# Kernel tuning notes

Hardware: AMD Instinct MI355X
Metric: run time of the kernel (lower is better)

The kernel has to match this reference:

```python
import jax, jax.numpy as jnp
import numpy as np

EPS = 1e-12
BETA = 0.25

def normalise(x, axis=-1):
    return x * jax.lax.rsqrt(jnp.mean(x * x, axis=axis, keepdims=True) + EPS)

def setup_inputs() -> dict:
    key = jax.random.key(0)
    ks = jax.random.split(key, 4)
    N, F, D, C = 8192, 512, 64, 8192
    return {
        "z": jax.random.normal(ks[0], (N, F), dtype=jnp.float32),
        "W_in": jax.random.normal(ks[1], (F, D), dtype=jnp.float32) * (1.0 / np.sqrt(F)),
        "b_in": jnp.zeros((D,), dtype=jnp.float32),
        "codebook": jax.random.normal(ks[2], (C, D), dtype=jnp.float32),
        "W_out": jax.random.normal(ks[3], (D, F), dtype=jnp.float32) * (1.0 / np.sqrt(D)),
        "b_out": jnp.zeros((F,), dtype=jnp.float32),
    }

def reference(z, W_in, b_in, codebook, W_out, b_out):
    sg = jax.lax.stop_gradient
    # input projection: [N, F] -> [N, D]
    zp = z @ W_in + b_in
    zn = normalise(zp)                  # [N, D]
    cn = normalise(codebook)            # [C, D]
    # squared euclidean distance via matmul expansion (same math as
    # sum((z[:,None]-c[None])**2, -1), avoids [N,C,D] materialization)
    z_sq = jnp.sum(zn * zn, axis=-1, keepdims=True)          # [N, 1]
    c_sq = jnp.sum(cn * cn, axis=-1)[None, :]                # [1, C]
    distance = z_sq + c_sq - 2.0 * (zn @ cn.T)               # [N, C]
    idxes = jnp.argmin(distance, axis=-1)                    # [N]
    codes = normalise(codebook[idxes], axis=-1)               # [N, D]
    loss = BETA * jnp.mean((sg(zn) - codes) ** 2) + jnp.mean((zn - sg(codes)) ** 2)
    codes = zn + sg(codes - zn)                               # straight-through
    out = codes @ W_out + b_out                               # [N, F]
    return (out, loss, idxes)
```

## Files before the change

kernel.cpp:

```cpp
#include <hip/hip_runtime.h>
#include <hip/hip_bf16.h>

#define N_ROWS 8192
#define F_DIM  512
#define D_DIM  64
#define C_CODES 8192

typedef __attribute__((ext_vector_type(8))) short bf16x8;
typedef __attribute__((ext_vector_type(4))) float f32x4;

__device__ __forceinline__ unsigned short rne_bf16(float x) {
  unsigned u = __float_as_uint(x);
  return (unsigned short)((u + 0x7FFFu + ((u >> 16) & 1u)) >> 16);
}
__device__ __forceinline__ float bf16_to_f(unsigned short u) {
  return __uint_as_float(((unsigned)u) << 16);
}
__device__ __forceinline__ void limb3(const float* xs, bf16x8& H, bf16x8& M, bf16x8& L) {
  #pragma unroll
  for (int j = 0; j < 8; ++j) {
    float x = xs[j];
    unsigned short h = rne_bf16(x);
    float r1 = x - bf16_to_f(h);
    unsigned short m = rne_bf16(r1);
    float r2 = r1 - bf16_to_f(m);
    unsigned short lo = rne_bf16(r2);
    H[j] = (short)h; M[j] = (short)m; L[j] = (short)lo;
  }
}

__global__ __launch_bounds__(256) void k_swz_win(
    const float* __restrict__ W, unsigned short* __restrict__ dst) {
  const int tid = threadIdx.x, w = tid >> 6, l = tid & 63;
  const int task = blockIdx.x * 4 + w;
  const int kc = task >> 2, cg = task & 3;
  const int lo = l & 15, hi = l >> 4;
  float xs[8];
  #pragma unroll
  for (int j = 0; j < 8; ++j)
    xs[j] = W[(size_t)(kc * 32 + hi * 8 + j) * D_DIM + cg * 16 + lo];
  bf16x8 H, M, L;
  limb3(xs, H, M, L);
  const int fb = (kc * 4 + cg) * 3;
  unsigned short* d0 = dst + (size_t)(fb + 0) * 512 + l * 8;
  unsigned short* d1 = dst + (size_t)(fb + 1) * 512 + l * 8;
  unsigned short* d2 = dst + (size_t)(fb + 2) * 512 + l * 8;
  #pragma unroll
  for (int j = 0; j < 8; ++j) { d0[j] = (unsigned short)H[j]; d1[j] = (unsigned short)M[j]; d2[j] = (unsigned short)L[j]; }
}

__global__ __launch_bounds__(256) void k_swz_wout(
    const float* __restrict__ W, unsigned short* __restrict__ dst) {
  const int tid = threadIdx.x, w = tid >> 6, l = tid & 63;
  const int task = blockIdx.x * 4 + w;
  const int cg = task >> 1, c = task & 1;
  const int lo = l & 15, hi = l >> 4;
  float xs[8];
  #pragma unroll
  for (int j = 0; j < 8; ++j)
    xs[j] = W[(size_t)(c * 32 + hi * 8 + j) * F_DIM + cg * 16 + lo];
  bf16x8 H, M, L;
  limb3(xs, H, M, L);
  const int fb = (cg * 2 + c) * 3;
  unsigned short* d0 = dst + (size_t)(fb + 0) * 512 + l * 8;
  unsigned short* d1 = dst + (size_t)(fb + 1) * 512 + l * 8;
  unsigned short* d2 = dst + (size_t)(fb + 2) * 512 + l * 8;
  #pragma unroll
  for (int j = 0; j < 8; ++j) { d0[j] = (unsigned short)H[j]; d1[j] = (unsigned short)M[j]; d2[j] = (unsigned short)L[j]; }
}

__global__ __launch_bounds__(256) void k_cn(
    const float* __restrict__ cb, float* __restrict__ cn,
    unsigned short* __restrict__ cn_sw) {
  const int tid = threadIdx.x, w = tid >> 6, l = tid & 63;
  const int g = blockIdx.x * 4 + w;
  const int lo = l & 15, hi = l >> 4;
  const int code = g * 16 + lo;

  float xs[2][8];
  float s = 0.0f;
  #pragma unroll
  for (int c = 0; c < 2; ++c) {
    const float* sp = cb + (size_t)code * D_DIM + c * 32 + hi * 8;
    float4 a = *(const float4*)sp, b = *(const float4*)(sp + 4);
    xs[c][0]=a.x; xs[c][1]=a.y; xs[c][2]=a.z; xs[c][3]=a.w;
    xs[c][4]=b.x; xs[c][5]=b.y; xs[c][6]=b.z; xs[c][7]=b.w;
    #pragma unroll
    for (int j = 0; j < 8; ++j) s += xs[c][j] * xs[c][j];
  }
  s += __shfl_xor(s, 16);
  s += __shfl_xor(s, 32);
  float inv = rsqrtf(s * (1.0f / 64.0f) + 1e-12f);

  #pragma unroll
  for (int c = 0; c < 2; ++c) {
    #pragma unroll
    for (int j = 0; j < 8; ++j) xs[c][j] *= inv;
    float* dp = cn + (size_t)code * D_DIM + c * 32 + hi * 8;
    *(float4*)dp = make_float4(xs[c][0], xs[c][1], xs[c][2], xs[c][3]);
    *(float4*)(dp + 4) = make_float4(xs[c][4], xs[c][5], xs[c][6], xs[c][7]);
    bf16x8 H, M, L;
    limb3(xs[c], H, M, L);
    const int fb = (g * 2 + c) * 3;
    unsigned short* d0 = cn_sw + (size_t)(fb + 0) * 512 + l * 8;
    unsigned short* d1 = cn_sw + (size_t)(fb + 1) * 512 + l * 8;
    unsigned short* d2 = cn_sw + (size_t)(fb + 2) * 512 + l * 8;
    #pragma unroll
    for (int j = 0; j < 8; ++j) { d0[j] = (unsigned short)H[j]; d1[j] = (unsigned short)M[j]; d2[j] = (unsigned short)L[j]; }
  }
}

__global__ __launch_bounds__(64) void k_zn(
    const float* __restrict__ z, const unsigned short* __restrict__ w_in_sw,
    const float* __restrict__ b_in, float* __restrict__ zn,
    unsigned short* __restrict__ zn_sw) {
  __shared__ float t_lds[16 * 65];
  const int l = threadIdx.x;
  const int lo = l & 15, hi = l >> 4;
  const int g = blockIdx.x;
  const int r0 = g * 16;
  const bf16x8* Bptr = (const bf16x8*)w_in_sw;
  const float* zbase = z + (size_t)(r0 + lo) * F_DIM + hi * 8;

  f32x4 acc[4];
  #pragma unroll
  for (int cg = 0; cg < 4; ++cg) acc[cg] = (f32x4){0.f, 0.f, 0.f, 0.f};

  bf16x8 Bu[12], Bv[12];
  #pragma unroll
  for (int i = 0; i < 12; ++i) Bu[i] = Bptr[(size_t)i * 64 + l];
  float4 za = *(const float4*)zbase;
  float4 zb = *(const float4*)(zbase + 4);

  #define ZSTEP(BCUR, BNXT, KC)                                               \
    {                                                                         \
      int kn = ((KC) < 15) ? (KC) + 1 : 15;                                   \
      float4 na = *(const float4*)(zbase + kn * 32);                          \
      float4 nb = *(const float4*)(zbase + kn * 32 + 4);                      \
      _Pragma("unroll")                                                       \
      for (int i = 0; i < 12; ++i)                                            \
        BNXT[i] = Bptr[((size_t)kn * 12 + i) * 64 + l];                       \
      float xs[8] = {za.x, za.y, za.z, za.w, zb.x, zb.y, zb.z, zb.w};         \
      bf16x8 Ah, Am, Al;                                                      \
      limb3(xs, Ah, Am, Al);                                                  \
      _Pragma("unroll")                                                       \
      for (int cg = 0; cg < 4; ++cg) {                                        \
        f32x4 t = acc[cg];                                                    \
        t = __builtin_amdgcn_mfma_f32_16x16x32_bf16(Ah, BCUR[cg*3+0], t, 0,0,0); \
        t = __builtin_amdgcn_mfma_f32_16x16x32_bf16(Ah, BCUR[cg*3+1], t, 0,0,0); \
        t = __builtin_amdgcn_mfma_f32_16x16x32_bf16(Am, BCUR[cg*3+0], t, 0,0,0); \
        t = __builtin_amdgcn_mfma_f32_16x16x32_bf16(Ah, BCUR[cg*3+2], t, 0,0,0); \
        t = __builtin_amdgcn_mfma_f32_16x16x32_bf16(Al, BCUR[cg*3+0], t, 0,0,0); \
        t = __builtin_amdgcn_mfma_f32_16x16x32_bf16(Am, BCUR[cg*3+1], t, 0,0,0); \
        acc[cg] = t;                                                          \
      }                                                                       \
      za = na; zb = nb;                                                       \
    }

  for (int kc = 0; kc < 16; kc += 2) {
    ZSTEP(Bu, Bv, kc)
    ZSTEP(Bv, Bu, kc + 1)
  }
  #undef ZSTEP

  #pragma unroll
  for (int r = 0; r < 4; ++r) {
    float v[4], s = 0.0f;
    #pragma unroll
    for (int cg = 0; cg < 4; ++cg) {
      v[cg] = acc[cg][r] + b_in[cg * 16 + lo];
      s += v[cg] * v[cg];
    }
    s += __shfl_xor(s, 1);
    s += __shfl_xor(s, 2);
    s += __shfl_xor(s, 4);
    s += __shfl_xor(s, 8);
    float inv = rsqrtf(s * (1.0f / 64.0f) + 1e-12f);
    #pragma unroll
    for (int cg = 0; cg < 4; ++cg)
      t_lds[(hi * 4 + r) * 65 + cg * 16 + lo] = v[cg] * inv;
  }
  __syncthreads();

  #pragma unroll
  for (int c = 0; c < 2; ++c) {
    float xs[8];
    #pragma unroll
    for (int j = 0; j < 8; ++j) xs[j] = t_lds[lo * 65 + c * 32 + hi * 8 + j];
    float* dp = zn + (size_t)(r0 + lo) * D_DIM + c * 32 + hi * 8;
    *(float4*)dp = make_float4(xs[0], xs[1], xs[2], xs[3]);
    *(float4*)(dp + 4) = make_float4(xs[4], xs[5], xs[6], xs[7]);
    bf16x8 H, M, L;
    limb3(xs, H, M, L);
    const int fb = (g * 2 + c) * 3;
    unsigned short* d0 = zn_sw + (size_t)(fb + 0) * 512 + l * 8;
    unsigned short* d1 = zn_sw + (size_t)(fb + 1) * 512 + l * 8;
    unsigned short* d2 = zn_sw + (size_t)(fb + 2) * 512 + l * 8;
    #pragma unroll
    for (int j = 0; j < 8; ++j) { d0[j] = (unsigned short)H[j]; d1[j] = (unsigned short)M[j]; d2[j] = (unsigned short)L[j]; }
  }
}

__global__ __launch_bounds__(256, 2) void k_argmax(
    const unsigned short* __restrict__ zn_sw,
    const unsigned short* __restrict__ cn_sw,
    float* __restrict__ pval, int* __restrict__ pidx) {
  const int tid = threadIdx.x;
  const int w = tid >> 6, l = tid & 63;
  const int lo = l & 15, hi = l >> 4;
  const int gA0 = (blockIdx.x * 4 + w) * 2;
  const int gB0 = blockIdx.y * 64;
  const bf16x8* Ab = (const bf16x8*)zn_sw;
  const bf16x8* Bb = (const bf16x8*)cn_sw;

  bf16x8 A0[2][3], A1[2][3];
  #pragma unroll
  for (int c = 0; c < 2; ++c)
    #pragma unroll
    for (int m = 0; m < 3; ++m) {
      A0[c][m] = Ab[(size_t)((gA0 * 2 + c) * 3 + m) * 64 + l];
      A1[c][m] = Ab[(size_t)(((gA0 + 1) * 2 + c) * 3 + m) * 64 + l];
    }

  bf16x8 Bu[2][3], Bv[2][3];
  #pragma unroll
  for (int c = 0; c < 2; ++c)
    #pragma unroll
    for (int m = 0; m < 3; ++m)
      Bu[c][m] = Bb[(size_t)((gB0 * 2 + c) * 3 + m) * 64 + l];

  float bv[8];
  int bi[8];
  #pragma unroll
  for (int i = 0; i < 8; ++i) { bv[i] = -1e30f; bi[i] = 0; }
  int cand = blockIdx.y * 1024 + lo;

  #define LOADB(dst, gB)                                                     \
    _Pragma("unroll")                                                        \
    for (int c = 0; c < 2; ++c)                                              \
      _Pragma("unroll")                                                      \
      for (int m = 0; m < 3; ++m)                                            \
        dst[c][m] = Bb[(size_t)(((gB) * 2 + c) * 3 + m) * 64 + l];

  #define COMPUTE(B)                                                          \
    {                                                                         \
      f32x4 a0 = {0.f,0.f,0.f,0.f}, a1 = {0.f,0.f,0.f,0.f};                   \
      f32x4 a2 = {0.f,0.f,0.f,0.f}, a3 = {0.f,0.f,0.f,0.f};                   \
      a0 = __builtin_amdgcn_mfma_f32_16x16x32_bf16(A0[0][0], B[0][0], a0, 0,0,0); \
      a1 = __builtin_amdgcn_mfma_f32_16x16x32_bf16(A0[1][0], B[1][0], a1, 0,0,0); \
      a2 = __builtin_amdgcn_mfma_f32_16x16x32_bf16(A1[0][0], B[0][0], a2, 0,0,0); \
      a3 = __builtin_amdgcn_mfma_f32_16x16x32_bf16(A1[1][0], B[1][0], a3, 0,0,0); \
      a0 = __builtin_amdgcn_mfma_f32_16x16x32_bf16(A0[0][0], B[0][1], a0, 0,0,0); \
      a1 = __builtin_amdgcn_mfma_f32_16x16x32_bf16(A0[1][0], B[1][1], a1, 0,0,0); \
      a2 = __builtin_amdgcn_mfma_f32_16x16x32_bf16(A1[0][0], B[0][1], a2, 0,0,0); \
      a3 = __builtin_amdgcn_mfma_f32_16x16x32_bf16(A1[1][0], B[1][1], a3, 0,0,0); \
      a0 = __builtin_amdgcn_mfma_f32_16x16x32_bf16(A0[0][1], B[0][0], a0, 0,0,0); \
      a1 = __builtin_amdgcn_mfma_f32_16x16x32_bf16(A0[1][1], B[1][0], a1, 0,0,0); \
      a2 = __builtin_amdgcn_mfma_f32_16x16x32_bf16(A1[0][1], B[0][0], a2, 0,0,0); \
      a3 = __builtin_amdgcn_mfma_f32_16x16x32_bf16(A1[1][1], B[1][0], a3, 0,0,0); \
      a0 = __builtin_amdgcn_mfma_f32_16x16x32_bf16(A0[0][0], B[0][2], a0, 0,0,0); \
      a1 = __builtin_amdgcn_mfma_f32_16x16x32_bf16(A0[1][0], B[1][2], a1, 0,0,0); \
      a2 = __builtin_amdgcn_mfma_f32_16x16x32_bf16(A1[0][0], B[0][2], a2, 0,0,0); \
      a3 = __builtin_amdgcn_mfma_f32_16x16x32_bf16(A1[1][0], B[1][2], a3, 0,0,0); \
      a0 = __builtin_amdgcn_mfma_f32_16x16x32_bf16(A0[0][2], B[0][0], a0, 0,0,0); \
      a1 = __builtin_amdgcn_mfma_f32_16x16x32_bf16(A0[1][2], B[1][0], a1, 0,0,0); \
      a2 = __builtin_amdgcn_mfma_f32_16x16x32_bf16(A1[0][2], B[0][0], a2, 0,0,0); \
      a3 = __builtin_amdgcn_mfma_f32_16x16x32_bf16(A1[1][2], B[1][0], a3, 0,0,0); \
      a0 = __builtin_amdgcn_mfma_f32_16x16x32_bf16(A0[0][1], B[0][1], a0, 0,0,0); \
      a1 = __builtin_amdgcn_mfma_f32_16x16x32_bf16(A0[1][1], B[1][1], a1, 0,0,0); \
      a2 = __builtin_amdgcn_mfma_f32_16x16x32_bf16(A1[0][1], B[0][1], a2, 0,0,0); \
      a3 = __builtin_amdgcn_mfma_f32_16x16x32_bf16(A1[1][1], B[1][1], a3, 0,0,0); \
      _Pragma("unroll")                                                       \
      for (int r = 0; r < 4; ++r) {                                           \
        float d0 = a0[r] + a1[r];                                             \
        if (d0 > bv[r]) { bv[r] = d0; bi[r] = cand; }                         \
        float d1 = a2[r] + a3[r];                                             \
        if (d1 > bv[4 + r]) { bv[4 + r] = d1; bi[4 + r] = cand; }             \
      }                                                                       \
      cand += 16;                                                             \
    }

  for (int p = 0; p < 64; p += 2) {
    LOADB(Bv, gB0 + p + 1);
    COMPUTE(Bu);
    LOADB(Bu, gB0 + p + 2);
    COMPUTE(Bv);
  }
  #undef LOADB
  #undef COMPUTE

  #pragma unroll
  for (int i = 0; i < 8; ++i) {
    float v = bv[i]; int ix = bi[i];
    #pragma unroll
    for (int m = 1; m < 16; m <<= 1) {
      float ov = __shfl_xor(v, m);
      int oi = __shfl_xor(ix, m);
      if (ov > v || (ov == v && oi < ix)) { v = ov; ix = oi; }
    }
    bv[i] = v; bi[i] = ix;
  }
  if (lo == 0) {
    int off = blockIdx.y * N_ROWS;
    int base0 = gA0 * 16 + hi * 4;
    int base1 = (gA0 + 1) * 16 + hi * 4;
    #pragma unroll
    for (int r = 0; r < 4; ++r) {
      pval[off + base0 + r] = bv[r];     pidx[off + base0 + r] = bi[r];
      pval[off + base1 + r] = bv[4 + r]; pidx[off + base1 + r] = bi[4 + r];
    }
  }
}

__global__ __launch_bounds__(64) void k_out(
    const float* __restrict__ cn, const float* __restrict__ zn,
    const float* __restrict__ pval, const int* __restrict__ pidx,
    const unsigned short* __restrict__ w_out_sw,
    const float* __restrict__ b_out, float* __restrict__ out,
    float* __restrict__ idx_f, float* __restrict__ pl) {
  const int l = threadIdx.x;
  const int lo = l & 15, hi = l >> 4;
  const int r0 = blockIdx.x * 16;
  const int row = r0 + lo;

  float v = pval[row];
  int ix = pidx[row];
  #pragma unroll
  for (int q = 1; q < 8; ++q) {
    float vq = pval[q * N_ROWS + row];
    int iq = pidx[q * N_ROWS + row];
    if (vq > v) { v = vq; ix = iq; }
  }
  if (hi == 0) idx_f[row] = (float)ix;

  bf16x8 A[2][3];
  float lp = 0.0f;
  #pragma unroll
  for (int c = 0; c < 2; ++c) {
    const float* cp = cn + (size_t)ix * D_DIM + c * 32 + hi * 8;
    const float* zp = zn + (size_t)row * D_DIM + c * 32 + hi * 8;
    float4 c0 = *(const float4*)cp, c1 = *(const float4*)(cp + 4);
    float4 z0 = *(const float4*)zp, z1 = *(const float4*)(zp + 4);
    float xs[8] = {c0.x, c0.y, c0.z, c0.w, c1.x, c1.y, c1.z, c1.w};
    float zs[8] = {z0.x, z0.y, z0.z, z0.w, z1.x, z1.y, z1.z, z1.w};
    limb3(xs, A[c][0], A[c][1], A[c][2]);
    #pragma unroll
    for (int j = 0; j < 8; ++j) { float d = xs[j] - zs[j]; lp += d * d; }
  }
  #pragma unroll
  for (int m = 1; m < 64; m <<= 1) lp += __shfl_xor(lp, m);
  if (l == 0) pl[blockIdx.x] = lp;

  const bf16x8* Bptr = (const bf16x8*)w_out_sw;
  bf16x8 Bu[6], Bv[6];
  #pragma unroll
  for (int i = 0; i < 6; ++i) Bu[i] = Bptr[(size_t)i * 64 + l];

  #define OSTEP(BCUR, BNXT, CG)                                               \
    {                                                                         \
      _Pragma("unroll")                                                       \
      for (int i = 0; i < 6; ++i)                                             \
        BNXT[i] = Bptr[((size_t)((CG) + 1) * 6 + i) * 64 + l];                \
      f32x4 a0 = {0.f,0.f,0.f,0.f}, a1 = {0.f,0.f,0.f,0.f};                   \
      a0 = __builtin_amdgcn_mfma_f32_16x16x32_bf16(A[0][0], BCUR[0], a0, 0,0,0); \
      a1 = __builtin_amdgcn_mfma_f32_16x16x32_bf16(A[1][0], BCUR[3], a1, 0,0,0); \
      a0 = __builtin_amdgcn_mfma_f32_16x16x32_bf16(A[0][0], BCUR[1], a0, 0,0,0); \
      a1 = __builtin_amdgcn_mfma_f32_16x16x32_bf16(A[1][0], BCUR[4], a1, 0,0,0); \
      a0 = __builtin_amdgcn_mfma_f32_16x16x32_bf16(A[0][1], BCUR[0], a0, 0,0,0); \
      a1 = __builtin_amdgcn_mfma_f32_16x16x32_bf16(A[1][1], BCUR[3], a1, 0,0,0); \
      a0 = __builtin_amdgcn_mfma_f32_16x16x32_bf16(A[0][0], BCUR[2], a0, 0,0,0); \
      a1 = __builtin_amdgcn_mfma_f32_16x16x32_bf16(A[1][0], BCUR[5], a1, 0,0,0); \
      a0 = __builtin_amdgcn_mfma_f32_16x16x32_bf16(A[0][2], BCUR[0], a0, 0,0,0); \
      a1 = __builtin_amdgcn_mfma_f32_16x16x32_bf16(A[1][2], BCUR[3], a1, 0,0,0); \
      a0 = __builtin_amdgcn_mfma_f32_16x16x32_bf16(A[0][1], BCUR[1], a0, 0,0,0); \
      a1 = __builtin_amdgcn_mfma_f32_16x16x32_bf16(A[1][1], BCUR[4], a1, 0,0,0); \
      float bb = b_out[(CG) * 16 + lo];                                       \
      _Pragma("unroll")                                                       \
      for (int r = 0; r < 4; ++r)                                             \
        out[(size_t)(r0 + hi * 4 + r) * F_DIM + (CG) * 16 + lo] =             \
            a0[r] + a1[r] + bb;                                               \
    }

  for (int cg = 0; cg < 32; cg += 2) {
    OSTEP(Bu, Bv, cg)
    OSTEP(Bv, Bu, cg + 1)
  }
  #undef OSTEP
}

__global__ __launch_bounds__(64) void k_loss_final(
    const float* __restrict__ pl, float* __restrict__ loss_out) {
  const int l = threadIdx.x;
  float s = 0.0f;
  #pragma unroll
  for (int i = 0; i < 8; ++i) s += pl[l + 64 * i];
  #pragma unroll
  for (int m = 1; m < 64; m <<= 1) s += __shfl_xor(s, m);
  if (l == 0) loss_out[0] = s * (1.25f / (float)(N_ROWS * D_DIM));
}

extern "C" void kernel_launch(void* const* d_in, const int* in_sizes, int n_in,
                              void* d_out, int out_size, void* d_ws, size_t ws_size,
                              hipStream_t stream) {
  const float* z        = (const float*)d_in[0];
  const float* W_in     = (const float*)d_in[1];
  const float* b_in     = (const float*)d_in[2];
  const float* codebook = (const float*)d_in[3];
  const float* W_out    = (const float*)d_in[4];
  const float* b_out    = (const float*)d_in[5];

  float* outp   = (float*)d_out;
  float* loss_f = outp + (size_t)N_ROWS * F_DIM;
  float* idx_f  = loss_f + 1;

  float* wsf = (float*)d_ws;
  float* zn_ws = wsf;
  float* cn_ws = wsf + 524288;
  unsigned short* zn_sw = (unsigned short*)(wsf + 1048576);
  unsigned short* cn_sw = (unsigned short*)(wsf + 1835008);
  unsigned short* win_sw  = (unsigned short*)(wsf + 2625536);
  unsigned short* wout_sw = (unsigned short*)(wsf + 2674688);
  float* pval_ws = wsf + 2723840;
  int*   pidx_ws = (int*)(wsf + 2789376);
  float* pl_ws   = wsf + 2854912;

  hipLaunchKernelGGL(k_swz_win, dim3(16), dim3(256), 0, stream, W_in, win_sw);
  hipLaunchKernelGGL(k_swz_wout, dim3(16), dim3(256), 0, stream, W_out, wout_sw);
  hipLaunchKernelGGL(k_cn, dim3(128), dim3(256), 0, stream,
                     codebook, cn_ws, cn_sw);
  hipLaunchKernelGGL(k_zn, dim3(512), dim3(64), 0, stream,
                     z, win_sw, b_in, zn_ws, zn_sw);
  hipLaunchKernelGGL(k_argmax, dim3(64, 8), dim3(256), 0, stream,
                     zn_sw, cn_sw, pval_ws, pidx_ws);
  hipLaunchKernelGGL(k_out, dim3(512), dim3(64), 0, stream,
                     cn_ws, zn_ws, pval_ws, pidx_ws, wout_sw, b_out,
                     outp, idx_f, pl_ws);
  hipLaunchKernelGGL(k_loss_final, dim3(1), dim3(64), 0, stream,
                     pl_ws, loss_f);
}
```

Baseline: 154.5 us.

## Merge prep kernels, split K and F across waves, double argmax code splits

```diff
diff --git a/kernel.cpp b/kernel.cpp
--- a/kernel.cpp
+++ b/kernel.cpp
@@ -29,96 +29,92 @@
   }
 }
 
-__global__ __launch_bounds__(256) void k_swz_win(
-    const float* __restrict__ W, unsigned short* __restrict__ dst) {
+__global__ __launch_bounds__(256) void k_prep(
+    const float* __restrict__ W_in, const float* __restrict__ W_out,
+    const float* __restrict__ cb,
+    unsigned short* __restrict__ win_sw, unsigned short* __restrict__ wout_sw,
+    float* __restrict__ cn, unsigned short* __restrict__ cn_sw) {
   const int tid = threadIdx.x, w = tid >> 6, l = tid & 63;
-  const int task = blockIdx.x * 4 + w;
-  const int kc = task >> 2, cg = task & 3;
   const int lo = l & 15, hi = l >> 4;
-  float xs[8];
-  #pragma unroll
-  for (int j = 0; j < 8; ++j)
-    xs[j] = W[(size_t)(kc * 32 + hi * 8 + j) * D_DIM + cg * 16 + lo];
-  bf16x8 H, M, L;
-  limb3(xs, H, M, L);
-  const int fb = (kc * 4 + cg) * 3;
-  unsigned short* d0 = dst + (size_t)(fb + 0) * 512 + l * 8;
-  unsigned short* d1 = dst + (size_t)(fb + 1) * 512 + l * 8;
-  unsigned short* d2 = dst + (size_t)(fb + 2) * 512 + l * 8;
-  #pragma unroll
-  for (int j = 0; j < 8; ++j) { d0[j] = (unsigned short)H[j]; d1[j] = (unsigned short)M[j]; d2[j] = (unsigned short)L[j]; }
-}
-
-__global__ __launch_bounds__(256) void k_swz_wout(
-    const float* __restrict__ W, unsigned short* __restrict__ dst) {
-  const int tid = threadIdx.x, w = tid >> 6, l = tid & 63;
-  const int task = blockIdx.x * 4 + w;
-  const int cg = task >> 1, c = task & 1;
-  const int lo = l & 15, hi = l >> 4;
-  float xs[8];
-  #pragma unroll
-  for (int j = 0; j < 8; ++j)
-    xs[j] = W[(size_t)(c * 32 + hi * 8 + j) * F_DIM + cg * 16 + lo];
-  bf16x8 H, M, L;
-  limb3(xs, H, M, L);
-  const int fb = (cg * 2 + c) * 3;
-  unsigned short* d0 = dst + (size_t)(fb + 0) * 512 + l * 8;
-  unsigned short* d1 = dst + (size_t)(fb + 1) * 512 + l * 8;
-  unsigned short* d2 = dst + (size_t)(fb + 2) * 512 + l * 8;
-  #pragma unroll
-  for (int j = 0; j < 8; ++j) { d0[j] = (unsigned short)H[j]; d1[j] = (unsigned short)M[j]; d2[j] = (unsigned short)L[j]; }
-}
-
-__global__ __launch_bounds__(256) void k_cn(
-    const float* __restrict__ cb, float* __restrict__ cn,
-    unsigned short* __restrict__ cn_sw) {
-  const int tid = threadIdx.x, w = tid >> 6, l = tid & 63;
-  const int g = blockIdx.x * 4 + w;
-  const int lo = l & 15, hi = l >> 4;
-  const int code = g * 16 + lo;
-
-  float xs[2][8];
-  float s = 0.0f;
-  #pragma unroll
-  for (int c = 0; c < 2; ++c) {
-    const float* sp = cb + (size_t)code * D_DIM + c * 32 + hi * 8;
-    float4 a = *(const float4*)sp, b = *(const float4*)(sp + 4);
-    xs[c][0]=a.x; xs[c][1]=a.y; xs[c][2]=a.z; xs[c][3]=a.w;
-    xs[c][4]=b.x; xs[c][5]=b.y; xs[c][6]=b.z; xs[c][7]=b.w;
-    #pragma unroll
-    for (int j = 0; j < 8; ++j) s += xs[c][j] * xs[c][j];
-  }
-  s += __shfl_xor(s, 16);
-  s += __shfl_xor(s, 32);
-  float inv = rsqrtf(s * (1.0f / 64.0f) + 1e-12f);
-
-  #pragma unroll
-  for (int c = 0; c < 2; ++c) {
-    #pragma unroll
-    for (int j = 0; j < 8; ++j) xs[c][j] *= inv;
-    float* dp = cn + (size_t)code * D_DIM + c * 32 + hi * 8;
-    *(float4*)dp = make_float4(xs[c][0], xs[c][1], xs[c][2], xs[c][3]);
-    *(float4*)(dp + 4) = make_float4(xs[c][4], xs[c][5], xs[c][6], xs[c][7]);
+  const int bid = blockIdx.x;
+
+  if (bid < 16) {
+    const int task = bid * 4 + w;
+    const int kc = task >> 2, cg = task & 3;
+    float xs[8];
+    #pragma unroll
+    for (int j = 0; j < 8; ++j)
+      xs[j] = W_in[(size_t)(kc * 32 + hi * 8 + j) * D_DIM + cg * 16 + lo];
     bf16x8 H, M, L;
-    limb3(xs[c], H, M, L);
-    const int fb = (g * 2 + c) * 3;
-    unsigned short* d0 = cn_sw + (size_t)(fb + 0) * 512 + l * 8;
-    unsigned short* d1 = cn_sw + (size_t)(fb + 1) * 512 + l * 8;
-    unsigned short* d2 = cn_sw + (size_t)(fb + 2) * 512 + l * 8;
+    limb3(xs, H, M, L);
+    const int fb = (kc * 4 + cg) * 3;
+    unsigned short* d0 = win_sw + (size_t)(fb + 0) * 512 + l * 8;
+    unsigned short* d1 = win_sw + (size_t)(fb + 1) * 512 + l * 8;
+    unsigned short* d2 = win_sw + (size_t)(fb + 2) * 512 + l * 8;
     #pragma unroll
     for (int j = 0; j < 8; ++j) { d0[j] = (unsigned short)H[j]; d1[j] = (unsigned short)M[j]; d2[j] = (unsigned short)L[j]; }
-  }
-}
-
-__global__ __launch_bounds__(64) void k_zn(
+  } else if (bid < 32) {
+    const int task = (bid - 16) * 4 + w;
+    const int cg = task >> 1, c = task & 1;
+    float xs[8];
+    #pragma unroll
+    for (int j = 0; j < 8; ++j)
+      xs[j] = W_out[(size_t)(c * 32 + hi * 8 + j) * F_DIM + cg * 16 + lo];
+    bf16x8 H, M, L;
+    limb3(xs, H, M, L);
+    const int fb = (cg * 2 + c) * 3;
+    unsigned short* d0 = wout_sw + (size_t)(fb + 0) * 512 + l * 8;
+    unsigned short* d1 = wout_sw + (size_t)(fb + 1) * 512 + l * 8;
+    unsigned short* d2 = wout_sw + (size_t)(fb + 2) * 512 + l * 8;
+    #pragma unroll
+    for (int j = 0; j < 8; ++j) { d0[j] = (unsigned short)H[j]; d1[j] = (unsigned short)M[j]; d2[j] = (unsigned short)L[j]; }
+  } else {
+    const int g = (bid - 32) * 4 + w;
+    const int code = g * 16 + lo;
+    float xs[2][8];
+    float s = 0.0f;
+    #pragma unroll
+    for (int c = 0; c < 2; ++c) {
+      const float* sp = cb + (size_t)code * D_DIM + c * 32 + hi * 8;
+      float4 a = *(const float4*)sp, b = *(const float4*)(sp + 4);
+      xs[c][0]=a.x; xs[c][1]=a.y; xs[c][2]=a.z; xs[c][3]=a.w;
+      xs[c][4]=b.x; xs[c][5]=b.y; xs[c][6]=b.z; xs[c][7]=b.w;
+      #pragma unroll
+      for (int j = 0; j < 8; ++j) s += xs[c][j] * xs[c][j];
+    }
+    s += __shfl_xor(s, 16);
+    s += __shfl_xor(s, 32);
+    float inv = rsqrtf(s * (1.0f / 64.0f) + 1e-12f);
+    #pragma unroll
+    for (int c = 0; c < 2; ++c) {
+      #pragma unroll
+      for (int j = 0; j < 8; ++j) xs[c][j] *= inv;
+      float* dp = cn + (size_t)code * D_DIM + c * 32 + hi * 8;
+      *(float4*)dp = make_float4(xs[c][0], xs[c][1], xs[c][2], xs[c][3]);
+      *(float4*)(dp + 4) = make_float4(xs[c][4], xs[c][5], xs[c][6], xs[c][7]);
+      bf16x8 H, M, L;
+      limb3(xs[c], H, M, L);
+      const int fb = (g * 2 + c) * 3;
+      unsigned short* d0 = cn_sw + (size_t)(fb + 0) * 512 + l * 8;
+      unsigned short* d1 = cn_sw + (size_t)(fb + 1) * 512 + l * 8;
+      unsigned short* d2 = cn_sw + (size_t)(fb + 2) * 512 + l * 8;
+      #pragma unroll
+      for (int j = 0; j < 8; ++j) { d0[j] = (unsigned short)H[j]; d1[j] = (unsigned short)M[j]; d2[j] = (unsigned short)L[j]; }
+    }
+  }
+}
+
+__global__ __launch_bounds__(256) void k_zn(
     const float* __restrict__ z, const unsigned short* __restrict__ w_in_sw,
     const float* __restrict__ b_in, float* __restrict__ zn,
     unsigned short* __restrict__ zn_sw) {
+  __shared__ float red[4096];
   __shared__ float t_lds[16 * 65];
-  const int l = threadIdx.x;
+  const int tid = threadIdx.x, w = tid >> 6, l = tid & 63;
   const int lo = l & 15, hi = l >> 4;
   const int g = blockIdx.x;
   const int r0 = g * 16;
+  const int kcb = w * 4;
   const bf16x8* Bptr = (const bf16x8*)w_in_sw;
   const float* zbase = z + (size_t)(r0 + lo) * F_DIM + hi * 8;
 
@@ -128,18 +124,12 @@
 
   bf16x8 Bu[12], Bv[12];
   #pragma unroll
-  for (int i = 0; i < 12; ++i) Bu[i] = Bptr[(size_t)i * 64 + l];
-  float4 za = *(const float4*)zbase;
-  float4 zb = *(const float4*)(zbase + 4);
-
-  #define ZSTEP(BCUR, BNXT, KC)                                               \
+  for (int i = 0; i < 12; ++i) Bu[i] = Bptr[((size_t)kcb * 12 + i) * 64 + l];
+  float4 za = *(const float4*)(zbase + kcb * 32);
+  float4 zb = *(const float4*)(zbase + kcb * 32 + 4);
+
+  #define ZMFMA(BCUR)                                                         \
     {                                                                         \
-      int kn = ((KC) < 15) ? (KC) + 1 : 15;                                   \
-      float4 na = *(const float4*)(zbase + kn * 32);                          \
-      float4 nb = *(const float4*)(zbase + kn * 32 + 4);                      \
-      _Pragma("unroll")                                                       \
-      for (int i = 0; i < 12; ++i)                                            \
-        BNXT[i] = Bptr[((size_t)kn * 12 + i) * 64 + l];                       \
       float xs[8] = {za.x, za.y, za.z, za.w, zb.x, zb.y, zb.z, zb.w};         \
       bf16x8 Ah, Am, Al;                                                      \
       limb3(xs, Ah, Am, Al);                                                  \
@@ -154,22 +144,50 @@
         t = __builtin_amdgcn_mfma_f32_16x16x32_bf16(Am, BCUR[cg*3+1], t, 0,0,0); \
         acc[cg] = t;                                                          \
       }                                                                       \
-      za = na; zb = nb;                                                       \
-    }
-
-  for (int kc = 0; kc < 16; kc += 2) {
-    ZSTEP(Bu, Bv, kc)
-    ZSTEP(Bv, Bu, kc + 1)
-  }
-  #undef ZSTEP
-
-  #pragma unroll
-  for (int r = 0; r < 4; ++r) {
+    }
+
+  {
+    float4 na = *(const float4*)(zbase + (kcb + 1) * 32);
+    float4 nb = *(const float4*)(zbase + (kcb + 1) * 32 + 4);
+    #pragma unroll
+    for (int i = 0; i < 12; ++i) Bv[i] = Bptr[((size_t)(kcb + 1) * 12 + i) * 64 + l];
+    ZMFMA(Bu)
+    za = na; zb = nb;
+  }
+  {
+    float4 na = *(const float4*)(zbase + (kcb + 2) * 32);
+    float4 nb = *(const float4*)(zbase + (kcb + 2) * 32 + 4);
+    #pragma unroll
+    for (int i = 0; i < 12; ++i) Bu[i] = Bptr[((size_t)(kcb + 2) * 12 + i) * 64 + l];
+    ZMFMA(Bv)
+    za = na; zb = nb;
+  }
+  {
+    float4 na = *(const float4*)(zbase + (kcb + 3) * 32);
+    float4 nb = *(const float4*)(zbase + (kcb + 3) * 32 + 4);
+    #pragma unroll
+    for (int i = 0; i < 12; ++i) Bv[i] = Bptr[((size_t)(kcb + 3) * 12 + i) * 64 + l];
+    ZMFMA(Bu)
+    za = na; zb = nb;
+  }
+  ZMFMA(Bv)
+  #undef ZMFMA
+
+  #pragma unroll
+  for (int cg = 0; cg < 4; ++cg)
+    #pragma unroll
+    for (int r = 0; r < 4; ++r)
+      red[((w * 4 + cg) * 4 + r) * 64 + l] = acc[cg][r];
+  __syncthreads();
+
+  {
     float v[4], s = 0.0f;
     #pragma unroll
     for (int cg = 0; cg < 4; ++cg) {
-      v[cg] = acc[cg][r] + b_in[cg * 16 + lo];
-      s += v[cg] * v[cg];
+      float t = b_in[cg * 16 + lo];
+      #pragma unroll
+      for (int w2 = 0; w2 < 4; ++w2) t += red[((w2 * 4 + cg) * 4 + w) * 64 + l];
+      v[cg] = t; s += t * t;
     }
     s += __shfl_xor(s, 1);
     s += __shfl_xor(s, 2);
@@ -178,12 +196,12 @@
     float inv = rsqrtf(s * (1.0f / 64.0f) + 1e-12f);
     #pragma unroll
     for (int cg = 0; cg < 4; ++cg)
-      t_lds[(hi * 4 + r) * 65 + cg * 16 + lo] = v[cg] * inv;
+      t_lds[(hi * 4 + w) * 65 + cg * 16 + lo] = v[cg] * inv;
   }
   __syncthreads();
 
-  #pragma unroll
-  for (int c = 0; c < 2; ++c) {
+  if (w < 2) {
+    const int c = w;
     float xs[8];
     #pragma unroll
     for (int j = 0; j < 8; ++j) xs[j] = t_lds[lo * 65 + c * 32 + hi * 8 + j];
@@ -201,7 +219,7 @@
   }
 }
 
-__global__ __launch_bounds__(256, 2) void k_argmax(
+__global__ __launch_bounds__(256, 4) void k_argmax(
     const unsigned short* __restrict__ zn_sw,
     const unsigned short* __restrict__ cn_sw,
     float* __restrict__ pval, int* __restrict__ pidx) {
@@ -209,7 +227,7 @@
   const int w = tid >> 6, l = tid & 63;
   const int lo = l & 15, hi = l >> 4;
   const int gA0 = (blockIdx.x * 4 + w) * 2;
-  const int gB0 = blockIdx.y * 64;
+  const int gB0 = blockIdx.y * 32;
   const bf16x8* Ab = (const bf16x8*)zn_sw;
   const bf16x8* Bb = (const bf16x8*)cn_sw;
 
@@ -233,7 +251,7 @@
   int bi[8];
   #pragma unroll
   for (int i = 0; i < 8; ++i) { bv[i] = -1e30f; bi[i] = 0; }
-  int cand = blockIdx.y * 1024 + lo;
+  int cand = blockIdx.y * 512 + lo;
 
   #define LOADB(dst, gB)                                                     \
     _Pragma("unroll")                                                        \
@@ -280,7 +298,7 @@
       cand += 16;                                                             \
     }
 
-  for (int p = 0; p < 64; p += 2) {
+  for (int p = 0; p < 32; p += 2) {
     LOADB(Bv, gB0 + p + 1);
     COMPUTE(Bu);
     LOADB(Bu, gB0 + p + 2);
@@ -312,13 +330,13 @@
   }
 }
 
-__global__ __launch_bounds__(64) void k_out(
+__global__ __launch_bounds__(256) void k_out(
     const float* __restrict__ cn, const float* __restrict__ zn,
     const float* __restrict__ pval, const int* __restrict__ pidx,
     const unsigned short* __restrict__ w_out_sw,
     const float* __restrict__ b_out, float* __restrict__ out,
     float* __restrict__ idx_f, float* __restrict__ pl) {
-  const int l = threadIdx.x;
+  const int tid = threadIdx.x, w = tid >> 6, l = tid & 63;
   const int lo = l & 15, hi = l >> 4;
   const int r0 = blockIdx.x * 16;
   const int row = r0 + lo;
@@ -326,12 +344,12 @@
   float v = pval[row];
   int ix = pidx[row];
   #pragma unroll
-  for (int q = 1; q < 8; ++q) {
+  for (int q = 1; q < 16; ++q) {
     float vq = pval[q * N_ROWS + row];
     int iq = pidx[q * N_ROWS + row];
     if (vq > v) { v = vq; ix = iq; }
   }
-  if (hi == 0) idx_f[row] = (float)ix;
+  if (w == 0 && hi == 0) idx_f[row] = (float)ix;
 
   bf16x8 A[2][3];
   float lp = 0.0f;
@@ -347,14 +365,17 @@
     #pragma unroll
     for (int j = 0; j < 8; ++j) { float d = xs[j] - zs[j]; lp += d * d; }
   }
-  #pragma unroll
-  for (int m = 1; m < 64; m <<= 1) lp += __shfl_xor(lp, m);
-  if (l == 0) pl[blockIdx.x] = lp;
+  if (w == 0) {
+    #pragma unroll
+    for (int m = 1; m < 64; m <<= 1) lp += __shfl_xor(lp, m);
+    if (l == 0) pl[blockIdx.x] = lp;
+  }
 
   const bf16x8* Bptr = (const bf16x8*)w_out_sw;
+  const int cgb = w * 8;
   bf16x8 Bu[6], Bv[6];
   #pragma unroll
-  for (int i = 0; i < 6; ++i) Bu[i] = Bptr[(size_t)i * 64 + l];
+  for (int i = 0; i < 6; ++i) Bu[i] = Bptr[((size_t)cgb * 6 + i) * 64 + l];
 
   #define OSTEP(BCUR, BNXT, CG)                                               \
     {                                                                         \
@@ -381,7 +402,7 @@
             a0[r] + a1[r] + bb;                                               \
     }
 
-  for (int cg = 0; cg < 32; cg += 2) {
+  for (int cg = cgb; cg < cgb + 8; cg += 2) {
     OSTEP(Bu, Bv, cg)
     OSTEP(Bv, Bu, cg + 1)
   }
@@ -421,18 +442,16 @@
   unsigned short* win_sw  = (unsigned short*)(wsf + 2625536);
   unsigned short* wout_sw = (unsigned short*)(wsf + 2674688);
   float* pval_ws = wsf + 2723840;
-  int*   pidx_ws = (int*)(wsf + 2789376);
-  float* pl_ws   = wsf + 2854912;
-
-  hipLaunchKernelGGL(k_swz_win, dim3(16), dim3(256), 0, stream, W_in, win_sw);
-  hipLaunchKernelGGL(k_swz_wout, dim3(16), dim3(256), 0, stream, W_out, wout_sw);
-  hipLaunchKernelGGL(k_cn, dim3(128), dim3(256), 0, stream,
-                     codebook, cn_ws, cn_sw);
-  hipLaunchKernelGGL(k_zn, dim3(512), dim3(64), 0, stream,
+  int*   pidx_ws = (int*)(wsf + 2854912);
+  float* pl_ws   = wsf + 2985984;
+
+  hipLaunchKernelGGL(k_prep, dim3(160), dim3(256), 0, stream,
+                     W_in, W_out, codebook, win_sw, wout_sw, cn_ws, cn_sw);
+  hipLaunchKernelGGL(k_zn, dim3(512), dim3(256), 0, stream,
                      z, win_sw, b_in, zn_ws, zn_sw);
-  hipLaunchKernelGGL(k_argmax, dim3(64, 8), dim3(256), 0, stream,
+  hipLaunchKernelGGL(k_argmax, dim3(64, 16), dim3(256), 0, stream,
                      zn_sw, cn_sw, pval_ws, pidx_ws);
-  hipLaunchKernelGGL(k_out, dim3(512), dim3(64), 0, stream,
+  hipLaunchKernelGGL(k_out, dim3(512), dim3(256), 0, stream,
                      cn_ws, zn_ws, pval_ws, pidx_ws, wout_sw, b_out,
                      outp, idx_f, pl_ws);
   hipLaunchKernelGGL(k_loss_final, dim3(1), dim3(64), 0, stream,
```

Result: no change. 153.2 us (-0.8%).
